# Kernel optimization log

Measured on AMD Instinct MI355X. Metric: run time of the kernel, lower is better.

The kernel has to match this reference:

```python
import jax, jax.numpy as jnp
import numpy as np

NUM_HEADS = 8
PW_GROUPS = 3 * NUM_HEADS  # grouped 1x1 conv groups


def _conv(x, w, groups):
    # x: [B, Cin, H, W], w: [Cout, Cin/groups, kh, kw]
    return jax.lax.conv_general_dilated(
        x, w, window_strides=(1, 1), padding='SAME',
        feature_group_count=groups,
        dimension_numbers=('NCHW', 'OIHW', 'NCHW'))


def setup_inputs() -> dict:
    key = jax.random.key(0)
    ks = jax.random.split(key, 12)
    dim, N, B = 512, 4096, 2
    C = dim // 2  # 256
    s = 0.02
    return {
        'x': jax.random.normal(ks[0], (B, N, dim), jnp.float32),
        'w_reduce': jax.random.normal(ks[1], (dim, C), jnp.float32) * s,
        'w_qkv': jax.random.normal(ks[2], (C, 3 * C), jnp.float32) * s,
        'dw0': jax.random.normal(ks[3], (3 * C, 1, 3, 3), jnp.float32) * s,
        'pw0': jax.random.normal(ks[4], (3 * C, 3 * C // PW_GROUPS, 1, 1), jnp.float32) * s,
        'dw1': jax.random.normal(ks[5], (3 * C, 1, 5, 5), jnp.float32) * s,
        'pw1': jax.random.normal(ks[6], (3 * C, 3 * C // PW_GROUPS, 1, 1), jnp.float32) * s,
        'dw2': jax.random.normal(ks[7], (3 * C, 1, 7, 7), jnp.float32) * s,
        'pw2': jax.random.normal(ks[8], (3 * C, 3 * C // PW_GROUPS, 1, 1), jnp.float32) * s,
        'w_reduce2': jax.random.normal(ks[9], (6 * dim, 3 * C), jnp.float32) * s,
        'w_proj': jax.random.normal(ks[10], (C, dim), jnp.float32) * s,
        'b_proj': jax.random.normal(ks[11], (dim,), jnp.float32) * s,
    }


def reference(x, w_reduce, w_qkv, dw0, pw0, dw1, pw1, dw2, pw2,
              w_reduce2, w_proj, b_proj):
    B, N, dim = x.shape
    Hn = NUM_HEADS
    x = x @ w_reduce                       # [B, N, C]
    C = x.shape[-1]
    hd = C // Hn
    scale = hd ** -0.5
    Hs = int(np.sqrt(N))                   # spatial side

    qkv = x @ w_qkv                        # [B, N, 3C]
    qkv_img = qkv.transpose(0, 2, 1).reshape(B, 3 * C, Hs, Hs)

    branches = [qkv_img]
    for dw, pw in ((dw0, pw0), (dw1, pw1), (dw2, pw2)):
        y = _conv(qkv_img, dw, groups=3 * C)      # depthwise
        y = _conv(y, pw, groups=PW_GROUPS)        # grouped 1x1
        branches.append(y)
    cat = jnp.concatenate(branches, axis=1)       # [B, 12C, Hs, Hs]
    cat = cat.reshape(B, 12 * C, N).transpose(0, 2, 1)  # [B, N, 6*dim]
    msq = cat @ w_reduce2                          # [B, N, 3C]

    qkv = msq.reshape(B, N, 3, Hn, hd).transpose(2, 0, 3, 1, 4)  # [3,B,H,N,hd]
    q, k, v = qkv[0], qkv[1], qkv[2]

    # chunked attention: 2 chunks of N//2 tokens, attention within each chunk
    Nc = N // 2
    qc = q.reshape(B, Hn, 2, Nc, hd)
    kc = k.reshape(B, Hn, 2, Nc, hd)
    vc = v.reshape(B, Hn, 2, Nc, hd)
    attn = jnp.einsum('bhcqd,bhckd->bhcqk', qc, kc) * scale
    attn = jax.nn.softmax(attn, axis=-1)
    out = jnp.einsum('bhcqk,bhckd->bhcqd', attn, vc)  # [B,H,2,Nc,hd]
    out = out.transpose(0, 2, 3, 1, 4).reshape(B, N, C)
    return out @ w_proj + b_proj                  # [B, N, dim]
```

## Files before the change

### kernel.cpp

```cpp
#include <hip/hip_runtime.h>
#include <hip/hip_bf16.h>

typedef __bf16 bf16x8 __attribute__((ext_vector_type(8)));
typedef __bf16 bf16x4v __attribute__((ext_vector_type(4)));
typedef float f32x4 __attribute__((ext_vector_type(4)));
typedef unsigned int u32x4 __attribute__((ext_vector_type(4)));

using bf16 = __hip_bfloat16;

__global__ __launch_bounds__(256) void k_cvt_bf16(const float* __restrict__ in,
                                                  bf16* __restrict__ out) {
  const int i = (blockIdx.x * 256 + threadIdx.x) * 4;
  float4 v = *reinterpret_cast<const float4*>(in + i);
  out[i + 0] = __float2bfloat16(v.x);
  out[i + 1] = __float2bfloat16(v.y);
  out[i + 2] = __float2bfloat16(v.z);
  out[i + 3] = __float2bfloat16(v.w);
}

__global__ __launch_bounds__(256) void k_transpose_bf16(const float* __restrict__ w,
                                                        bf16* __restrict__ wt,
                                                        int K, int N) {
  __shared__ float t[32][33];
  const int k0 = blockIdx.x * 32, n0 = blockIdx.y * 32;
  const int tx = threadIdx.x & 31, ty = threadIdx.x >> 5;
#pragma unroll
  for (int i = 0; i < 32; i += 8)
    t[ty + i][tx] = w[(size_t)(k0 + ty + i) * N + n0 + tx];
  __syncthreads();
#pragma unroll
  for (int i = 0; i < 32; i += 8)
    wt[(size_t)(n0 + ty + i) * K + k0 + tx] = __float2bfloat16(t[tx][ty + i]);
}

__global__ __launch_bounds__(256) void k_transpose2d(const bf16* __restrict__ in,
                                                     bf16* __restrict__ out,
                                                     int R, int C) {
  __shared__ unsigned short tl[64][65];
  const int c0 = blockIdx.x * 64, r0 = blockIdx.y * 64;
  const size_t zb = (size_t)blockIdx.z * R * C;
  const int tx = threadIdx.x & 63, ty = threadIdx.x >> 6;
  const unsigned short* ip = (const unsigned short*)in + zb;
  unsigned short* op = (unsigned short*)out + zb;
#pragma unroll
  for (int i = 0; i < 64; i += 4)
    tl[ty + i][tx] = ip[(size_t)(r0 + ty + i) * C + c0 + tx];
  __syncthreads();
#pragma unroll
  for (int i = 0; i < 64; i += 4)
    op[(size_t)(c0 + ty + i) * R + r0 + tx] = tl[tx][ty + i];
}

__global__ __launch_bounds__(256) void k_gemm_bt(
    const bf16* __restrict__ A0, const bf16* __restrict__ A1,
    const bf16* __restrict__ A2, const bf16* __restrict__ A3,
    const bf16* __restrict__ Bt, bf16* __restrict__ Cb,
    float* __restrict__ Cf, const float* __restrict__ bias,
    int N, int K, int srcK, int split_bk) {
  __shared__ __align__(16) bf16 As[2][128 * 64];
  __shared__ __align__(16) bf16 Bs[2][128 * 64];
  const int tid = threadIdx.x;
  const int lane = tid & 63;
  const int wv = tid >> 6;
  const size_t M0 = (size_t)blockIdx.x * 128;
  const int N0 = blockIdx.y * 128;
  const int wr = (wv >> 1) * 64, wc = (wv & 1) * 64;
  const int fr = lane & 15, fo = (lane >> 4) * 8;
  const int lrow = lane >> 3, lcol = (lane & 7) << 3;
  f32x4 acc[4][4] = {};

  auto stage = [&](int kt, int buf) {
    const int s = kt / split_bk;
    const bf16* __restrict__ Ak = (s == 0) ? A0 : (s == 1) ? A1 : (s == 2) ? A2 : A3;
    const size_t aofs = (size_t)(kt - s * split_bk) * 64;
    const size_t bofs = (size_t)kt * 64;
#pragma unroll
    for (int ld = 0; ld < 4; ++ld) {
      const int row = wv * 32 + ld * 8 + lrow;
      const bf16* ga = Ak + (M0 + row) * (size_t)srcK + aofs + lcol;
      __builtin_amdgcn_global_load_lds(
          (const __attribute__((address_space(1))) unsigned int*)ga,
          (__attribute__((address_space(3))) unsigned int*)(As[buf] + (wv * 32 + ld * 8) * 64),
          16, 0, 0);
      const bf16* gb = Bt + (size_t)(N0 + row) * K + bofs + lcol;
      __builtin_amdgcn_global_load_lds(
          (const __attribute__((address_space(1))) unsigned int*)gb,
          (__attribute__((address_space(3))) unsigned int*)(Bs[buf] + (wv * 32 + ld * 8) * 64),
          16, 0, 0);
    }
  };

  const int nsteps = K >> 6;
  stage(0, 0);
  __syncthreads();
  int cur = 0;
  for (int kt = 0; kt < nsteps; ++kt) {
    if (kt + 1 < nsteps) stage(kt + 1, cur ^ 1);
#pragma unroll
    for (int kk = 0; kk < 64; kk += 32) {
      bf16x8 a[4], b[4];
#pragma unroll
      for (int m = 0; m < 4; ++m)
        a[m] = *reinterpret_cast<const bf16x8*>(As[cur] + (wr + m * 16 + fr) * 64 + kk + fo);
#pragma unroll
      for (int n = 0; n < 4; ++n)
        b[n] = *reinterpret_cast<const bf16x8*>(Bs[cur] + (wc + n * 16 + fr) * 64 + kk + fo);
#pragma unroll
      for (int m = 0; m < 4; ++m)
#pragma unroll
        for (int n = 0; n < 4; ++n)
          acc[m][n] = __builtin_amdgcn_mfma_f32_16x16x32_bf16(a[m], b[n], acc[m][n], 0, 0, 0);
    }
    __syncthreads();
    cur ^= 1;
  }

  const int rb = (lane >> 4) * 4;
#pragma unroll
  for (int m = 0; m < 4; ++m) {
#pragma unroll
    for (int n = 0; n < 4; ++n) {
      const size_t row = M0 + wr + m * 16 + rb;
      const int col = N0 + wc + n * 16 + fr;
      if (Cb != nullptr) {
#pragma unroll
        for (int r = 0; r < 4; ++r)
          Cb[(row + r) * N + col] = __float2bfloat16(acc[m][n][r]);
      } else {
        const float bb = bias[col];
#pragma unroll
        for (int r = 0; r < 4; ++r)
          Cf[(row + r) * N + col] = acc[m][n][r] + bb;
      }
    }
  }
}

template <int KS>
__global__ __launch_bounds__(256) void k_dwconv_img(const bf16* __restrict__ in,
                                                    const float* __restrict__ w,
                                                    bf16* __restrict__ out) {
  constexpr int P = KS / 2;
  constexpr int ROWS = 64 + 2 * P;
  constexpr int PITCH = 80;
  constexpr int NCHUNK = ROWS * PITCH * 2 / 16;
  __shared__ __align__(16) bf16 pl[ROWS * PITCH];
  const int t = threadIdx.x;
  const int c = blockIdx.x, b = blockIdx.y;
  const bf16* __restrict__ ip = in + ((size_t)b * 768 + c) * 4096;
  bf16* __restrict__ op = out + ((size_t)b * 768 + c) * 4096;

  u32x4* pl4 = reinterpret_cast<u32x4*>(pl);
  for (int i = t; i < NCHUNK; i += 256) pl4[i] = u32x4{0, 0, 0, 0};
  __syncthreads();
  for (int q = t; q < 512; q += 256) {
    const int px0 = q * 8;
    const int y = px0 >> 6, x = px0 & 63;
    u32x4 v = *reinterpret_cast<const u32x4*>(ip + px0);
    *reinterpret_cast<u32x4*>(&pl[(y + P) * PITCH + 8 + x]) = v;
  }
  __syncthreads();

  float wk[KS * KS];
#pragma unroll
  for (int i = 0; i < KS * KS; ++i) wk[i] = w[c * KS * KS + i];

  const int x = t & 63;
  const int y0 = (t >> 6) * 16;
  float win[KS][KS];
#pragma unroll
  for (int r = 0; r < 2 * P; ++r)
#pragma unroll
    for (int kx = 0; kx < KS; ++kx)
      win[r % KS][kx] = __bfloat162float(pl[(y0 + r) * PITCH + 8 + x - P + kx]);
#pragma unroll
  for (int yy = 0; yy < 16; ++yy) {
    constexpr int twoP = 2 * P;
#pragma unroll
    for (int kx = 0; kx < KS; ++kx)
      win[(yy + twoP) % KS][kx] =
          __bfloat162float(pl[(y0 + yy + twoP) * PITCH + 8 + x - P + kx]);
    float acc = 0.f;
#pragma unroll
    for (int ky = 0; ky < KS; ++ky)
#pragma unroll
      for (int kx = 0; kx < KS; ++kx)
        acc += win[(yy + ky) % KS][kx] * wk[ky * KS + kx];
    op[(y0 + yy) * 64 + x] = __float2bfloat16(acc);
  }
}

__global__ __launch_bounds__(256) void k_pwconv_img(const bf16* __restrict__ in,
                                                    const float* __restrict__ w,
                                                    bf16* __restrict__ out) {
  const int co0 = blockIdx.x * 4;
  const int g = co0 >> 5;
  const int b = blockIdx.z;
  const int px = blockIdx.y * 2048 + threadIdx.x * 8;
  const bf16* __restrict__ ip = in + ((size_t)b * 768 + g * 32) * 4096 + px;
  float acc[4][8] = {};
#pragma unroll
  for (int ci = 0; ci < 32; ++ci) {
    const bf16x8 v = *reinterpret_cast<const bf16x8*>(ip + (size_t)ci * 4096);
    float fv[8];
#pragma unroll
    for (int j = 0; j < 8; ++j) fv[j] = (float)v[j];
#pragma unroll
    for (int q = 0; q < 4; ++q) {
      const float wq = w[(co0 + q) * 32 + ci];
#pragma unroll
      for (int j = 0; j < 8; ++j) acc[q][j] += wq * fv[j];
    }
  }
#pragma unroll
  for (int q = 0; q < 4; ++q) {
    bf16x8 o;
#pragma unroll
    for (int j = 0; j < 8; ++j) o[j] = (__bf16)acc[q][j];
    *reinterpret_cast<bf16x8*>(out + ((size_t)b * 768 + co0 + q) * 4096 + px) = o;
  }
}

__global__ __launch_bounds__(256) void k_attn(const bf16* __restrict__ msq,
                                              bf16* __restrict__ out) {
  const int qt = blockIdx.x;
  const int combo = blockIdx.y;
  const int b = combo >> 4;
  const int h = (combo >> 1) & 7;
  const int ck = combo & 1;
  const int tid = threadIdx.x, lane = tid & 63, wv = tid >> 6;
  const int fr = lane & 15, hi = lane >> 4, fo = hi * 8;
  const size_t base = (size_t)b * 4096 * 768;
  const int n0 = ck * 2048 + qt * 128;

  __shared__ __align__(16) bf16 Kl[64][40];
  __shared__ __align__(16) bf16 Vt[32][72];
  __shared__ __align__(16) bf16 Pl[4][2][16][72];

  const float scale = 0.17677669529663687f;
  bf16x8 qf[2];
#pragma unroll
  for (int t = 0; t < 2; ++t) {
    const int qrow = n0 + t * 64 + wv * 16 + fr;
    const bf16x8 v =
        *reinterpret_cast<const bf16x8*>(msq + base + (size_t)qrow * 768 + h * 32 + fo);
#pragma unroll
    for (int j = 0; j < 8; ++j) qf[t][j] = (__bf16)((float)v[j] * scale);
  }

  f32x4 oacc[2][2] = {};
  float mrun[2] = {-1e30f, -1e30f};
  float lrun[2] = {0.f, 0.f};
  const int sr = tid >> 2, sdc = (tid & 3) << 3;

  for (int kt = 0; kt < 32; ++kt) {
    const int m0 = ck * 2048 + kt * 64;
    __syncthreads();
    {
      const size_t rbase = base + (size_t)(m0 + sr) * 768 + h * 32;
      u32x4 kv = *reinterpret_cast<const u32x4*>(msq + rbase + 256 + sdc);
      *reinterpret_cast<u32x4*>(&Kl[sr][sdc]) = kv;
      u32x4 vvv = *reinterpret_cast<const u32x4*>(msq + rbase + 512 + sdc);
      const bf16* vp = reinterpret_cast<const bf16*>(&vvv);
#pragma unroll
      for (int j = 0; j < 8; ++j) Vt[sdc + j][sr] = vp[j];
    }
    __syncthreads();

    bf16x8 kf[4];
#pragma unroll
    for (int j = 0; j < 4; ++j)
      kf[j] = *reinterpret_cast<const bf16x8*>(&Kl[j * 16 + fr][fo]);

#pragma unroll
    for (int t = 0; t < 2; ++t) {
      f32x4 sacc[4];
#pragma unroll
      for (int j = 0; j < 4; ++j) {
        const f32x4 z = {0.f, 0.f, 0.f, 0.f};
        sacc[j] = __builtin_amdgcn_mfma_f32_16x16x32_bf16(kf[j], qf[t], z, 0, 0, 0);
      }
      float mx = -1e30f;
#pragma unroll
      for (int j = 0; j < 4; ++j)
#pragma unroll
        for (int r = 0; r < 4; ++r) mx = fmaxf(mx, sacc[j][r]);
      mx = fmaxf(mx, __shfl_xor(mx, 16));
      mx = fmaxf(mx, __shfl_xor(mx, 32));
      const float mnew = fmaxf(mrun[t], mx);
      const float corr = __expf(mrun[t] - mnew);
      mrun[t] = mnew;
      float sm = 0.f;
#pragma unroll
      for (int j = 0; j < 4; ++j) {
        bf16x4v pk;
#pragma unroll
        for (int r = 0; r < 4; ++r) {
          const float pz = __expf(sacc[j][r] - mnew);
          sm += pz;
          pk[r] = (__bf16)pz;
        }
        *reinterpret_cast<bf16x4v*>(&Pl[wv][t][fr][j * 16 + hi * 4]) = pk;
      }
      sm += __shfl_xor(sm, 16);
      sm += __shfl_xor(sm, 32);
      lrun[t] = lrun[t] * corr + sm;
#pragma unroll
      for (int r = 0; r < 4; ++r) {
        const float cf = __shfl(corr, hi * 4 + r);
        oacc[t][0][r] *= cf;
        oacc[t][1][r] *= cf;
      }
    }

#pragma unroll
    for (int t = 0; t < 2; ++t)
#pragma unroll
      for (int kk = 0; kk < 2; ++kk) {
        const bf16x8 pa = *reinterpret_cast<const bf16x8*>(&Pl[wv][t][fr][kk * 32 + fo]);
#pragma unroll
        for (int nb = 0; nb < 2; ++nb) {
          const bf16x8 vb = *reinterpret_cast<const bf16x8*>(&Vt[nb * 16 + fr][kk * 32 + fo]);
          oacc[t][nb] = __builtin_amdgcn_mfma_f32_16x16x32_bf16(pa, vb, oacc[t][nb], 0, 0, 0);
        }
      }
  }

#pragma unroll
  for (int t = 0; t < 2; ++t)
#pragma unroll
    for (int r = 0; r < 4; ++r) {
      const float lf = __shfl(lrun[t], hi * 4 + r);
      const float inv = 1.f / lf;
      const int row = n0 + t * 64 + wv * 16 + hi * 4 + r;
#pragma unroll
      for (int nb = 0; nb < 2; ++nb)
        out[((size_t)b * 4096 + row) * 256 + h * 32 + nb * 16 + fr] =
            __float2bfloat16(oacc[t][nb][r] * inv);
    }
}

extern "C" void kernel_launch(void* const* d_in, const int* in_sizes, int n_in,
                              void* d_out, int out_size, void* d_ws, size_t ws_size,
                              hipStream_t stream) {
  (void)in_sizes; (void)n_in; (void)out_size; (void)ws_size;
  const float* x    = (const float*)d_in[0];
  const float* wrd  = (const float*)d_in[1];
  const float* wqkv = (const float*)d_in[2];
  const float* dw0  = (const float*)d_in[3];
  const float* pw0  = (const float*)d_in[4];
  const float* dw1  = (const float*)d_in[5];
  const float* pw1  = (const float*)d_in[6];
  const float* dw2  = (const float*)d_in[7];
  const float* pw2  = (const float*)d_in[8];
  const float* wrd2 = (const float*)d_in[9];
  const float* wprj = (const float*)d_in[10];
  const float* bprj = (const float*)d_in[11];
  float* out = (float*)d_out;

  char* p = (char*)d_ws;
  auto nxt = [&](size_t bytes) {
    char* r = p;
    p += (bytes + 255) & ~(size_t)255;
    return (bf16*)r;
  };
  bf16* xb   = nxt(8192ull * 512 * 2);
  bf16* xr   = nxt(8192ull * 256 * 2);
  bf16* qkvT = xb;
  bf16* wrT  = nxt(256ull * 512 * 2);
  bf16* wqT  = nxt(768ull * 256 * 2);
  bf16* wr2T = nxt(768ull * 3072 * 2);
  bf16* wpT  = nxt(512ull * 256 * 2);
  bf16* qkv  = nxt(8192ull * 768 * 2);
  bf16* dtmp = nxt(8192ull * 768 * 2);
  bf16* y0   = nxt(8192ull * 768 * 2);
  bf16* y1   = nxt(8192ull * 768 * 2);
  bf16* y2   = nxt(8192ull * 768 * 2);
  bf16* msq  = nxt(8192ull * 768 * 2);
  bf16* pwT  = msq;
  bf16* ao   = nxt(8192ull * 256 * 2);

  k_cvt_bf16<<<(8192 * 512 / 4) / 256, 256, 0, stream>>>(x, xb);
  k_transpose_bf16<<<dim3(512 / 32, 256 / 32), 256, 0, stream>>>(wrd, wrT, 512, 256);
  k_transpose_bf16<<<dim3(256 / 32, 768 / 32), 256, 0, stream>>>(wqkv, wqT, 256, 768);
  k_transpose_bf16<<<dim3(3072 / 32, 768 / 32), 256, 0, stream>>>(wrd2, wr2T, 3072, 768);
  k_transpose_bf16<<<dim3(256 / 32, 512 / 32), 256, 0, stream>>>(wprj, wpT, 256, 512);

  k_gemm_bt<<<dim3(64, 2), 256, 0, stream>>>(xb, xb, xb, xb, wrT, xr, nullptr, nullptr,
                                             256, 512, 512, 1 << 20);
  k_gemm_bt<<<dim3(64, 6), 256, 0, stream>>>(xr, xr, xr, xr, wqT, qkv, nullptr, nullptr,
                                             768, 256, 256, 1 << 20);

  k_transpose2d<<<dim3(12, 64, 2), 256, 0, stream>>>(qkv, qkvT, 4096, 768);

  k_dwconv_img<3><<<dim3(768, 2), 256, 0, stream>>>(qkvT, dw0, dtmp);
  k_pwconv_img<<<dim3(192, 2, 2), 256, 0, stream>>>(dtmp, pw0, pwT);
  k_transpose2d<<<dim3(64, 12, 2), 256, 0, stream>>>(pwT, y0, 768, 4096);

  k_dwconv_img<5><<<dim3(768, 2), 256, 0, stream>>>(qkvT, dw1, dtmp);
  k_pwconv_img<<<dim3(192, 2, 2), 256, 0, stream>>>(dtmp, pw1, pwT);
  k_transpose2d<<<dim3(64, 12, 2), 256, 0, stream>>>(pwT, y1, 768, 4096);

  k_dwconv_img<7><<<dim3(768, 2), 256, 0, stream>>>(qkvT, dw2, dtmp);
  k_pwconv_img<<<dim3(192, 2, 2), 256, 0, stream>>>(dtmp, pw2, pwT);
  k_transpose2d<<<dim3(64, 12, 2), 256, 0, stream>>>(pwT, y2, 768, 4096);

  k_gemm_bt<<<dim3(64, 6), 256, 0, stream>>>(qkv, y0, y1, y2, wr2T, msq, nullptr, nullptr,
                                             768, 3072, 768, 12);

  k_attn<<<dim3(16, 32), 256, 0, stream>>>(msq, ao);

  k_gemm_bt<<<dim3(64, 4), 256, 0, stream>>>(ao, ao, ao, ao, wpT, nullptr, out, bprj,
                                             512, 256, 256, 1 << 20);
}
```

Measured before the change: 380.3 us.

## Double-buffer K/V tiles in attention kernel with register prefetch

The attention kernel now keeps two LDS buffers for the K and transposed V tiles. It issues the global loads for the next key tile into registers before computing on the current tile, then writes them to the other buffer afterwards. This removes one barrier per iteration and lets global memory latency overlap with the MFMA and softmax work. In exchange it doubles K/V shared memory and holds extra prefetch registers, which may reduce occupancy.

```diff
diff --git a/kernel.cpp b/kernel.cpp
--- a/kernel.cpp
+++ b/kernel.cpp
@@ -233,8 +233,8 @@
   const size_t base = (size_t)b * 4096 * 768;
   const int n0 = ck * 2048 + qt * 128;
 
-  __shared__ __align__(16) bf16 Kl[64][40];
-  __shared__ __align__(16) bf16 Vt[32][72];
+  __shared__ __align__(16) bf16 Kl[2][64][40];
+  __shared__ __align__(16) bf16 Vt[2][32][72];
   __shared__ __align__(16) bf16 Pl[4][2][16][72];
 
   const float scale = 0.17677669529663687f;
@@ -253,24 +253,30 @@
   float lrun[2] = {0.f, 0.f};
   const int sr = tid >> 2, sdc = (tid & 3) << 3;
 
+  u32x4 kr, vr;
+  auto gload = [&](int kt) {
+    const size_t rbase = base + (size_t)(ck * 2048 + kt * 64 + sr) * 768 + h * 32;
+    kr = *reinterpret_cast<const u32x4*>(msq + rbase + 256 + sdc);
+    vr = *reinterpret_cast<const u32x4*>(msq + rbase + 512 + sdc);
+  };
+  auto lwrite = [&](int buf) {
+    *reinterpret_cast<u32x4*>(&Kl[buf][sr][sdc]) = kr;
+    const bf16* vp = reinterpret_cast<const bf16*>(&vr);
+#pragma unroll
+    for (int j = 0; j < 8; ++j) Vt[buf][sdc + j][sr] = vp[j];
+  };
+
+  gload(0);
+  lwrite(0);
+  int cur = 0;
   for (int kt = 0; kt < 32; ++kt) {
-    const int m0 = ck * 2048 + kt * 64;
     __syncthreads();
-    {
-      const size_t rbase = base + (size_t)(m0 + sr) * 768 + h * 32;
-      u32x4 kv = *reinterpret_cast<const u32x4*>(msq + rbase + 256 + sdc);
-      *reinterpret_cast<u32x4*>(&Kl[sr][sdc]) = kv;
-      u32x4 vvv = *reinterpret_cast<const u32x4*>(msq + rbase + 512 + sdc);
-      const bf16* vp = reinterpret_cast<const bf16*>(&vvv);
-#pragma unroll
-      for (int j = 0; j < 8; ++j) Vt[sdc + j][sr] = vp[j];
-    }
-    __syncthreads();
+    if (kt + 1 < 32) gload(kt + 1);
 
     bf16x8 kf[4];
 #pragma unroll
     for (int j = 0; j < 4; ++j)
-      kf[j] = *reinterpret_cast<const bf16x8*>(&Kl[j * 16 + fr][fo]);
+      kf[j] = *reinterpret_cast<const bf16x8*>(&Kl[cur][j * 16 + fr][fo]);
 
 #pragma unroll
     for (int t = 0; t < 2; ++t) {
@@ -320,10 +326,14 @@
         const bf16x8 pa = *reinterpret_cast<const bf16x8*>(&Pl[wv][t][fr][kk * 32 + fo]);
 #pragma unroll
         for (int nb = 0; nb < 2; ++nb) {
-          const bf16x8 vb = *reinterpret_cast<const bf16x8*>(&Vt[nb * 16 + fr][kk * 32 + fo]);
+          const bf16x8 vb =
+              *reinterpret_cast<const bf16x8*>(&Vt[cur][nb * 16 + fr][kk * 32 + fo]);
           oacc[t][nb] = __builtin_amdgcn_mfma_f32_16x16x32_bf16(pa, vb, oacc[t][nb], 0, 0, 0);
         }
       }
+
+    if (kt + 1 < 32) lwrite(cur ^ 1);
+    cur ^= 1;
   }
 
 #pragma unroll
```

Result: no change. 375.2 us (-1.3%).
